# Kernel tuning notes

Hardware: AMD Instinct MI355X
Metric: run time of the kernel (lower is better)

Reference implementation:

```python
import jax, jax.numpy as jnp
import numpy as np

B, T, D, H, L, V = 2, 2048, 1024, 16, 12, 50257
HD = D // H          # head size 64
F = 4 * D            # FFN hidden 4096
EPS = 1e-5


def setup_inputs() -> dict:
    key = jax.random.key(0)
    keys = iter(jax.random.split(key, 16))
    n = lambda shape: jax.random.normal(next(keys), shape, jnp.float32) * 0.02
    inp = {
        "x": jax.random.randint(next(keys), (B, T), 0, V),
        "tok_emb": n((V, D)),
        "pos_emb": n((T, D)),
        "ln1_g": jnp.ones((L, D), jnp.float32), "ln1_b": jnp.zeros((L, D), jnp.float32),
        "wq": n((L, D, D)), "bq": jnp.zeros((L, D), jnp.float32),
        "wk": n((L, D, D)), "bk": jnp.zeros((L, D), jnp.float32),
        "wv": n((L, D, D)), "bv": jnp.zeros((L, D), jnp.float32),
        "wo": n((L, D, D)), "bo": jnp.zeros((L, D), jnp.float32),
        "ln2_g": jnp.ones((L, D), jnp.float32), "ln2_b": jnp.zeros((L, D), jnp.float32),
        "w1": n((L, D, F)), "b1": jnp.zeros((L, F), jnp.float32),
        "w2": n((L, F, D)), "b2": jnp.zeros((L, D), jnp.float32),
        "lnf_g": jnp.ones((D,), jnp.float32), "lnf_b": jnp.zeros((D,), jnp.float32),
        "fc_w": n((D, V)), "fc_b": jnp.zeros((V,), jnp.float32),
    }
    return inp


def _layernorm(x, g, b):
    m = jnp.mean(x, axis=-1, keepdims=True)
    v = jnp.var(x, axis=-1, keepdims=True)
    return (x - m) * jax.lax.rsqrt(v + EPS) * g + b


def _forward(x, tok_emb, pos_emb, ln1_g, ln1_b, wq, bq, wk, bk, wv, bv,
             wo, bo, ln2_g, ln2_b, w1, b1, w2, b2, lnf_g, lnf_b, fc_w, fc_b):
    # token + positional embedding (dropout is eval-mode identity)
    h = tok_emb[x] + pos_emb[None]                      # [B,T,D]
    mask = jnp.tril(jnp.ones((T, T), bool))             # causal mask
    scale = HD ** (-0.5)
    for l in range(L):
        # NOTE: original Block applies residual around the POST-norm activation
        hn = _layernorm(h, ln1_g[l], ln1_b[l])
        q = (hn @ wq[l] + bq[l]).reshape(B, T, H, HD)
        k = (hn @ wk[l] + bk[l]).reshape(B, T, H, HD)
        v = (hn @ wv[l] + bv[l]).reshape(B, T, H, HD)
        scores = jnp.einsum('bthd,bshd->bhts', q, k) * scale
        scores = jnp.where(mask[None, None], scores, -jnp.inf)
        attn = jax.nn.softmax(scores, axis=-1)
        o = jnp.einsum('bhts,bshd->bthd', attn, v).reshape(B, T, D)
        h = hn + (o @ wo[l] + bo[l])
        hn2 = _layernorm(h, ln2_g[l], ln2_b[l])
        h = hn2 + (jax.nn.relu(hn2 @ w1[l] + b1[l]) @ w2[l] + b2[l])
    h = _layernorm(h, lnf_g, lnf_b)
    logits = h @ fc_w + fc_b                            # [B,T,V]
    return logits


def reference(x, tok_emb, pos_emb, ln1_g, ln1_b, wq, bq, wk, bk, wv, bv,
              wo, bo, ln2_g, ln2_b, w1, b1, w2, b2, lnf_g, lnf_b, fc_w, fc_b):
    return _forward(x, tok_emb, pos_emb, ln1_g, ln1_b, wq, bq, wk, bk, wv, bv,
                    wo, bo, ln2_g, ln2_b, w1, b1, w2, b2, lnf_g, lnf_b, fc_w, fc_b)
```

## Files before the change

kernel.cpp:

```cpp
#include <hip/hip_runtime.h>

#define BB 2
#define TT 2048
#define DD 1024
#define HH 16
#define LL 12
#define VV 50257
#define VP 50432
#define HDD 64
#define FF 4096
#define MM (BB*TT)
#define QS 3072

typedef __bf16 bf16;
typedef __bf16 bf16x8 __attribute__((ext_vector_type(8)));
typedef __bf16 bf16x4 __attribute__((ext_vector_type(4)));
typedef __bf16 bf16x2 __attribute__((ext_vector_type(2)));
typedef float  f32x4  __attribute__((ext_vector_type(4)));
typedef float  f32x4u __attribute__((ext_vector_type(4), aligned(4)));
typedef unsigned int u32x4 __attribute__((ext_vector_type(4)));

typedef const __attribute__((address_space(1))) void* gas_t;
typedef __attribute__((address_space(3))) void* las_t;

__global__ __launch_bounds__(256) void k_embed(const int* __restrict__ x,
    const float* __restrict__ tok, const float* __restrict__ pos,
    float* __restrict__ h)
{
    int row = blockIdx.x;
    int t   = row & (TT - 1);
    int idx = x[row];
    int c   = threadIdx.x * 4;
    float4 a = *(const float4*)(tok + (size_t)idx * DD + c);
    float4 p = *(const float4*)(pos + (size_t)t   * DD + c);
    a.x += p.x; a.y += p.y; a.z += p.z; a.w += p.w;
    *(float4*)(h + (size_t)row * DD + c) = a;
}

__global__ __launch_bounds__(256) void k_ln(const float* __restrict__ in,
    const float* __restrict__ g, const float* __restrict__ b,
    float* __restrict__ outf, bf16* __restrict__ outb)
{
    int row = blockIdx.x, tid = threadIdx.x;
    const float4 v = *(const float4*)(in + (size_t)row * DD + tid * 4);
    float s  = v.x + v.y + v.z + v.w;
    float s2 = v.x*v.x + v.y*v.y + v.z*v.z + v.w*v.w;
    #pragma unroll
    for (int d = 1; d < 64; d <<= 1) { s += __shfl_xor(s, d); s2 += __shfl_xor(s2, d); }
    __shared__ float red[8];
    __shared__ float mv[2];
    int wid = tid >> 6, lane = tid & 63;
    if (lane == 0) { red[2*wid] = s; red[2*wid+1] = s2; }
    __syncthreads();
    if (tid == 0) {
        float ts  = red[0] + red[2] + red[4] + red[6];
        float ts2 = red[1] + red[3] + red[5] + red[7];
        float mean = ts * (1.0f / DD);
        float var  = ts2 * (1.0f / DD) - mean * mean;
        mv[0] = mean; mv[1] = 1.0f / sqrtf(var + 1e-5f);
    }
    __syncthreads();
    float mean = mv[0], inv = mv[1];
    float4 gg = *(const float4*)(g + tid * 4);
    float4 bb = *(const float4*)(b + tid * 4);
    float o0 = (v.x - mean) * inv * gg.x + bb.x;
    float o1 = (v.y - mean) * inv * gg.y + bb.y;
    float o2 = (v.z - mean) * inv * gg.z + bb.z;
    float o3 = (v.w - mean) * inv * gg.w + bb.w;
    size_t o = (size_t)row * DD + tid * 4;
    if (outf) { float4 r = {o0, o1, o2, o3}; *(float4*)(outf + o) = r; }
    if (outb) {
        bf16x4 r4 = {(bf16)o0, (bf16)o1, (bf16)o2, (bf16)o3};
        *(bf16x4*)(outb + o) = r4;
    }
}

__global__ __launch_bounds__(256) void k_wtrans(
    const float* __restrict__ src, bf16* __restrict__ dst,
    int K, int N, int Npad, size_t srcLS, size_t dstLS)
{
    src += (size_t)blockIdx.z * srcLS;
    dst += (size_t)blockIdx.z * dstLS;
    int k0 = blockIdx.y * 32, n0 = blockIdx.x * 256;
    __shared__ float tile[32][256];
    int tid = threadIdx.x;
    #pragma unroll
    for (int p = 0; p < 8; p++) {
        int kk = p * 4 + (tid >> 6);
        int nn = (tid & 63) * 4;
        const float* sp = src + (size_t)(k0 + kk) * N + n0 + nn;
        f32x4u v = {0.f, 0.f, 0.f, 0.f};
        if (n0 + nn + 3 < N) {
            v = *(const f32x4u*)sp;
        } else {
            #pragma unroll
            for (int i = 0; i < 4; i++)
                if (n0 + nn + i < N) v[i] = sp[i];
        }
        *(f32x4*)&tile[kk][nn] = v;
    }
    __syncthreads();
    int n = n0 + tid;
    if (n < Npad) {
        bf16 rowv[32];
        #pragma unroll
        for (int kk = 0; kk < 32; kk++) rowv[kk] = (bf16)tile[kk][tid];
        bf16* dp = dst + (size_t)n * K + k0;
        #pragma unroll
        for (int s = 0; s < 4; s++)
            *(bf16x8*)(dp + s * 8) = *(const bf16x8*)&rowv[s * 8];
    }
}

__global__ __launch_bounds__(256) void k_biasmerge(
    const float* __restrict__ bq, const float* __restrict__ bk,
    const float* __restrict__ bv, float* __restrict__ dst)
{
    int i = blockIdx.x * 256 + threadIdx.x;
    if (i >= LL * QS) return;
    int l = i / QS, j = i % QS;
    float v = (j < 1024) ? bq[l*1024 + j]
            : (j < 2048) ? bk[l*1024 + j - 1024]
                         : bv[l*1024 + j - 2048];
    dst[i] = v;
}

#define GEMM_EPILOGUE(MI_CNT, WM_STRIDE)                                        \
    bool nalign = ((Nout & 3) == 0);                                            \
    _Pragma("unroll")                                                           \
    for (int mi = 0; mi < MI_CNT; mi++) {                                       \
        int row = m0 + wm*WM_STRIDE + mi*16 + r16;                              \
        _Pragma("unroll")                                                       \
        for (int ni = 0; ni < 4; ni++) {                                        \
            int col0 = n0 + wn*64 + ni*16 + g4*4;                               \
            f32x4 v = acc[mi][ni];                                              \
            float sc = (qpre && col0 < 1024) ? 0.125f : 1.0f;                   \
            if (col0 + 3 < Nout) {                                              \
                if (bias) {                                                     \
                    float4 bi = *(const float4*)(bias + col0);                  \
                    v[0] += bi.x; v[1] += bi.y; v[2] += bi.z; v[3] += bi.w;     \
                }                                                               \
                if (res) {                                                      \
                    float4 rr = *(const float4*)(res + (size_t)row*Nout + col0);\
                    v[0] += rr.x; v[1] += rr.y; v[2] += rr.z; v[3] += rr.w;     \
                }                                                               \
                if (relu) { _Pragma("unroll")                                   \
                    for (int j = 0; j < 4; j++) v[j] = fmaxf(v[j], 0.0f); }     \
                if (outf) {                                                     \
                    float* p = outf + (size_t)row * Nout + col0;                \
                    if (nalign) *(f32x4*)p = v; else *(f32x4u*)p = v;           \
                }                                                               \
                if (outb) {                                                     \
                    bf16x4 o4 = {(bf16)(v[0]*sc), (bf16)(v[1]*sc),              \
                                 (bf16)(v[2]*sc), (bf16)(v[3]*sc)};             \
                    *(bf16x4*)(outb + (size_t)row * Nout + col0) = o4;          \
                }                                                               \
            } else {                                                            \
                _Pragma("unroll")                                               \
                for (int j = 0; j < 4; j++) {                                   \
                    int col = col0 + j;                                         \
                    if (col >= Nout) continue;                                  \
                    float vv = v[j] + (bias ? bias[col] : 0.0f);                \
                    if (res)  vv += res[(size_t)row * Nout + col];              \
                    if (relu) vv = fmaxf(vv, 0.0f);                             \
                    if (outf) outf[(size_t)row * Nout + col] = vv;              \
                    if (outb) outb[(size_t)row * Nout + col] = (bf16)(vv*sc);   \
                }                                                               \
            }                                                                   \
        }                                                                       \
    }


#define STG2(nn, kk)                                                            \
    do { const int k0_ = (nn)*64 + (kk)*32; const int db_ = (nn)&1;             \
        _Pragma("unroll") for (int i_ = 0; i_ < 2; i_++) {                      \
            int a_ = i_*2048 + tid*8;                                           \
            int sr_ = a_>>6, x_ = (a_&63) ^ ((sr_&7)<<3);                       \
            int r_ = 2*sr_ + (x_>>5), e_ = x_&31;                               \
            __builtin_amdgcn_global_load_lds(                                   \
                (gas_t)(A + (size_t)(m0+r_)*K + k0_+e_),                        \
                (las_t)&lA[db_][kk][a_], 16, 0, 0);                             \
        }                                                                       \
        _Pragma("unroll") for (int i_ = 0; i_ < 2; i_++) {                      \
            int a_ = i_*2048 + tid*8;                                           \
            int sr_ = a_>>6, x_ = (a_&63) ^ ((sr_&7)<<3);                       \
            int r_ = 2*sr_ + (x_>>5), e_ = x_&31;                               \
            __builtin_amdgcn_global_load_lds(                                   \
                (gas_t)(BT + (size_t)(n0+r_)*K + k0_+e_),                       \
                (las_t)&lB[db_][kk][a_], 16, 0, 0);                             \
        }                                                                       \
    } while (0)

#define PH2(nn, kk, sn, sk, wv)                                                 \
    { const int db_ = (nn)&1;                                                   \
        bf16x8 af[4], bfr[4];                                                   \
        _Pragma("unroll") for (int mi = 0; mi < 4; mi++) {                      \
            int row_ = wm*64 + mi*16 + r16;                                     \
            int sr_ = row_>>1;                                                  \
            int xp_ = (((row_&1)<<5) | kfrag) ^ ((sr_&7)<<3);                   \
            af[mi] = *(const bf16x8*)&lA[db_][kk][sr_*64 + xp_];                \
        }                                                                       \
        _Pragma("unroll") for (int ni = 0; ni < 4; ni++) {                      \
            int row_ = wn*64 + ni*16 + r16;                                     \
            int sr_ = row_>>1;                                                  \
            int xp_ = (((row_&1)<<5) | kfrag) ^ ((sr_&7)<<3);                   \
            bfr[ni] = *(const bf16x8*)&lB[db_][kk][sr_*64 + xp_];               \
        }                                                                       \
        bool st_ = (sn) < nt;                                                   \
        if (st_) STG2(sn, sk);                                                  \
        __builtin_amdgcn_sched_barrier(0);                                      \
        __builtin_amdgcn_s_barrier();                                           \
        __builtin_amdgcn_s_setprio(1);                                          \
        _Pragma("unroll") for (int mi = 0; mi < 4; mi++)                        \
            _Pragma("unroll") for (int ni = 0; ni < 4; ni++)                    \
                acc[mi][ni] = __builtin_amdgcn_mfma_f32_16x16x32_bf16(          \
                    bfr[ni], af[mi], acc[mi][ni], 0, 0, 0);                     \
        __builtin_amdgcn_s_setprio(0);                                          \
        if (wv) { if (st_) asm volatile("s_waitcnt vmcnt(4)" ::: "memory");     \
                  else     asm volatile("s_waitcnt vmcnt(0)" ::: "memory"); }   \
        __builtin_amdgcn_sched_barrier(0);                                      \
        __builtin_amdgcn_s_barrier();                                           \
    }

__global__ __launch_bounds__(256) void k_gemm2(
    const bf16* __restrict__ A, const bf16* __restrict__ BT,
    const float* __restrict__ bias, const float* __restrict__ res,
    float* __restrict__ outf, bf16* __restrict__ outb,
    int K, int Nout, int relu, int mswap, int qpre)
{
    __shared__ alignas(16) bf16 lA[2][2][128 * 32];
    __shared__ alignas(16) bf16 lB[2][2][128 * 32];
    int tid = threadIdx.x;
    int lane = tid & 63, w = tid >> 6;
    int wm = w >> 1, wn = w & 1;
    int nb = mswap ? blockIdx.y : blockIdx.x;
    int mb = mswap ? blockIdx.x : blockIdx.y;
    int n0 = nb * 128, m0 = mb * 128;
    int r16 = lane & 15, g4 = lane >> 4;
    int kfrag = g4 * 8;

    f32x4 acc[4][4];
    const f32x4 fzero = {0.f, 0.f, 0.f, 0.f};
    #pragma unroll
    for (int i = 0; i < 4; i++)
        #pragma unroll
        for (int j = 0; j < 4; j++) acc[i][j] = fzero;

    int nt = K >> 6;
    STG2(0, 0); STG2(0, 1); STG2(1, 0);
    asm volatile("s_waitcnt vmcnt(4)" ::: "memory");
    __builtin_amdgcn_sched_barrier(0);
    __builtin_amdgcn_s_barrier();
    for (int it2 = 0; it2 < nt; it2 += 2) {
        PH2(it2,     0, it2 + 1, 1, 0);
        PH2(it2,     1, it2 + 2, 0, 1);
        PH2(it2 + 1, 0, it2 + 2, 1, 0);
        PH2(it2 + 1, 1, it2 + 3, 0, 1);
    }
    GEMM_EPILOGUE(4, 64)
}

#define STG3(nn, kk)                                                            \
    do { const int k0_ = (nn)*64 + (kk)*32; const int db_ = (nn)&1;             \
        _Pragma("unroll") for (int i_ = 0; i_ < 2; i_++) {                      \
            int a_ = i_*4096 + tid*8;                                           \
            int sr_ = a_>>6, x_ = (a_&63) ^ ((sr_&7)<<3);                       \
            int r_ = 2*sr_ + (x_>>5), e_ = x_&31;                               \
            __builtin_amdgcn_global_load_lds(                                   \
                (gas_t)(A + (size_t)(m0+r_)*K + k0_+e_),                        \
                (las_t)&lA[db_][kk][a_], 16, 0, 0);                             \
        }                                                                       \
        _Pragma("unroll") for (int i_ = 0; i_ < 2; i_++) {                      \
            int a_ = i_*4096 + tid*8;                                           \
            int sr_ = a_>>6, x_ = (a_&63) ^ ((sr_&7)<<3);                       \
            int r_ = 2*sr_ + (x_>>5), e_ = x_&31;                               \
            __builtin_amdgcn_global_load_lds(                                   \
                (gas_t)(BT + (size_t)(n0+r_)*K + k0_+e_),                       \
                (las_t)&lB[db_][kk][a_], 16, 0, 0);                             \
        }                                                                       \
    } while (0)

#define PH3(nn, kk, sn, sk, wv)                                                 \
    { const int db_ = (nn)&1;                                                   \
        bf16x8 af[8], bfr[4];                                                   \
        _Pragma("unroll") for (int mi = 0; mi < 8; mi++) {                      \
            int row_ = wm*128 + mi*16 + r16;                                    \
            int sr_ = row_>>1;                                                  \
            int xp_ = (((row_&1)<<5) | kfrag) ^ ((sr_&7)<<3);                   \
            af[mi] = *(const bf16x8*)&lA[db_][kk][sr_*64 + xp_];                \
        }                                                                       \
        _Pragma("unroll") for (int ni = 0; ni < 4; ni++) {                      \
            int row_ = wn*64 + ni*16 + r16;                                     \
            int sr_ = row_>>1;                                                  \
            int xp_ = (((row_&1)<<5) | kfrag) ^ ((sr_&7)<<3);                   \
            bfr[ni] = *(const bf16x8*)&lB[db_][kk][sr_*64 + xp_];               \
        }                                                                       \
        bool st_ = (sn) < nt;                                                   \
        if (st_) STG3(sn, sk);                                                  \
        __builtin_amdgcn_sched_barrier(0);                                      \
        __builtin_amdgcn_s_barrier();                                           \
        __builtin_amdgcn_s_setprio(1);                                          \
        _Pragma("unroll") for (int mi = 0; mi < 8; mi++)                        \
            _Pragma("unroll") for (int ni = 0; ni < 4; ni++)                    \
                acc[mi][ni] = __builtin_amdgcn_mfma_f32_16x16x32_bf16(          \
                    bfr[ni], af[mi], acc[mi][ni], 0, 0, 0);                     \
        __builtin_amdgcn_s_setprio(0);                                          \
        if (wv) { if (st_) asm volatile("s_waitcnt vmcnt(4)" ::: "memory");     \
                  else     asm volatile("s_waitcnt vmcnt(0)" ::: "memory"); }   \
        __builtin_amdgcn_sched_barrier(0);                                      \
        __builtin_amdgcn_s_barrier();                                           \
    }

__global__ __launch_bounds__(512, 2) void k_gemm3(
    const bf16* __restrict__ A, const bf16* __restrict__ BT,
    const float* __restrict__ bias, const float* __restrict__ res,
    float* __restrict__ outf, bf16* __restrict__ outb,
    int K, int Nout, int relu, int mswap, int qpre)
{
    __shared__ alignas(16) bf16 lA[2][2][256 * 32];
    __shared__ alignas(16) bf16 lB[2][2][256 * 32];
    int tid = threadIdx.x;
    int lane = tid & 63, w = tid >> 6;
    int wm = w >> 2, wn = w & 3;
    int nb = mswap ? blockIdx.y : blockIdx.x;
    int mb = mswap ? blockIdx.x : blockIdx.y;
    int n0 = nb * 256, m0 = mb * 256;
    int r16 = lane & 15, g4 = lane >> 4;
    int kfrag = g4 * 8;

    f32x4 acc[8][4];
    const f32x4 fzero = {0.f, 0.f, 0.f, 0.f};
    #pragma unroll
    for (int i = 0; i < 8; i++)
        #pragma unroll
        for (int j = 0; j < 4; j++) acc[i][j] = fzero;

    int nt = K >> 6;
    STG3(0, 0); STG3(0, 1); STG3(1, 0);
    asm volatile("s_waitcnt vmcnt(4)" ::: "memory");
    __builtin_amdgcn_sched_barrier(0);
    __builtin_amdgcn_s_barrier();
    for (int it2 = 0; it2 < nt; it2 += 2) {
        PH3(it2,     0, it2 + 1, 1, 0);
        PH3(it2,     1, it2 + 2, 0, 1);
        PH3(it2 + 1, 0, it2 + 2, 1, 0);
        PH3(it2 + 1, 1, it2 + 3, 0, 1);
    }
    GEMM_EPILOGUE(8, 128)
}

__global__ __launch_bounds__(256) void k_gemm_f32b(
    const bf16* __restrict__ A, const float* __restrict__ Bm,
    const float* __restrict__ bias, float* __restrict__ outf,
    int M, int N, int K)
{
    __shared__ alignas(16) bf16 lA[128][40];
    __shared__ alignas(16) bf16 lB[128][40];
    int tid  = threadIdx.x;
    int lane = tid & 63, wid = tid >> 6;
    int wm = wid >> 1, wn = wid & 1;
    int m0 = blockIdx.x * 128, n0 = blockIdx.y * 128;
    int r16 = lane & 15, g4 = lane >> 4;

    f32x4 acc[4][4];
    const f32x4 fzero = {0.f, 0.f, 0.f, 0.f};
    #pragma unroll
    for (int i = 0; i < 4; i++)
        #pragma unroll
        for (int j = 0; j < 4; j++) acc[i][j] = fzero;

    int arow = tid >> 2, aseg = tid & 3;
    int bkr  = tid >> 3, bnb  = tid & 7;
    bool nfull = (n0 + 128 <= N);

    for (int k0 = 0; k0 < K; k0 += 32) {
        *(uint4*)&lA[arow][aseg*8] =
            *(const uint4*)(A + (size_t)(m0 + arow) * K + k0 + aseg*8);
        *(uint4*)&lA[arow + 64][aseg*8] =
            *(const uint4*)(A + (size_t)(m0 + arow + 64) * K + k0 + aseg*8);
        const float* bsrc = Bm + (size_t)(k0 + bkr) * N + n0;
        #pragma unroll
        for (int q = 0; q < 4; q++) {
            int n = q*32 + bnb*4;
            #pragma unroll
            for (int i = 0; i < 4; i++) {
                float fv = 0.0f;
                if (nfull || (n0 + n + i < N)) fv = bsrc[n + i];
                lB[n+i][bkr] = (bf16)fv;
            }
        }
        __syncthreads();
        int kb = g4 * 8;
        bf16x8 af[4], bfr[4];
        #pragma unroll
        for (int mi = 0; mi < 4; mi++)
            af[mi] = *(const bf16x8*)&lA[wm*64 + mi*16 + r16][kb];
        #pragma unroll
        for (int ni = 0; ni < 4; ni++)
            bfr[ni] = *(const bf16x8*)&lB[wn*64 + ni*16 + r16][kb];
        #pragma unroll
        for (int mi = 0; mi < 4; mi++)
            #pragma unroll
            for (int ni = 0; ni < 4; ni++)
                acc[mi][ni] = __builtin_amdgcn_mfma_f32_16x16x32_bf16(
                    af[mi], bfr[ni], acc[mi][ni], 0, 0, 0);
        __syncthreads();
    }

    #pragma unroll
    for (int ni = 0; ni < 4; ni++) {
        int col = n0 + wn*64 + ni*16 + r16;
        if (col >= N) continue;
        float bi = bias[col];
        #pragma unroll
        for (int mi = 0; mi < 4; mi++) {
            #pragma unroll
            for (int j = 0; j < 4; j++) {
                int row = m0 + wm*64 + mi*16 + g4*4 + j;
                outf[(size_t)row * N + col] = acc[mi][ni][j] + bi;
            }
        }
    }
}

__global__ __launch_bounds__(512) void k_attn3(
    const bf16* __restrict__ qkv, bf16* __restrict__ o)
{
    __shared__ alignas(16) bf16 lK[64][72];
    __shared__ alignas(16) bf16 lVT[64][72];
    int tid = threadIdx.x, lane = tid & 63, w = tid >> 6;
    int r16 = lane & 15, g4 = lane >> 4;
    int t0 = blockIdx.x * 128;
    int bh = blockIdx.y, bb = bh >> 4, hh = bh & 15;
    const bf16* base = qkv + (size_t)bb * TT * QS + hh * HDD;
    const bf16* kp = base + 1024;
    const bf16* vp = base + 2048;
    bf16* op = o + (size_t)bb * TT * DD + hh * HDD;
    int qrow = t0 + w * 16;

    bf16x8 qf0, qf1;
    {
        const bf16* qr = base + (size_t)(qrow + r16) * QS + g4 * 8;
        qf0 = *(const bf16x8*)qr;
        qf1 = *(const bf16x8*)(qr + 32);
    }

    int krow = tid >> 3, kseg = tid & 7;
    int vsp  = tid >> 4, vseg = tid & 15;

    f32x4 oacc[4];
    const f32x4 fzero = {0.f, 0.f, 0.f, 0.f};
    #pragma unroll
    for (int i = 0; i < 4; i++) oacc[i] = fzero;
    float mrun = -1e30f, lrun = 0.f;

    int send = t0 + 128;
    bf16x8 kr;
    bf16x4 va4, vb4;
    {
        kr  = *(const bf16x8*)(kp + (size_t)krow * QS + kseg * 8);
        va4 = *(const bf16x4*)(vp + (size_t)(2*vsp) * QS + vseg * 4);
        vb4 = *(const bf16x4*)(vp + (size_t)(2*vsp) * QS + QS + vseg * 4);
    }

    for (int s0 = 0; s0 < send; s0 += 64) {
        __syncthreads();
        *(bf16x8*)&lK[krow][kseg*8] = kr;
        #pragma unroll
        for (int i = 0; i < 4; i++) {
            int d = vseg*4 + i;
            int mpr = (vsp >> 2) ^ (d >> 3);
            bf16x2 pv2 = {va4[i], vb4[i]};
            *(unsigned int*)&lVT[d][mpr*8 + (vsp&3)*2] =
                __builtin_bit_cast(unsigned int, pv2);
        }
        if (s0 + 64 < send) {
            kr  = *(const bf16x8*)(kp + (size_t)(s0 + 64 + krow) * QS + kseg * 8);
            va4 = *(const bf16x4*)(vp + (size_t)(s0 + 64 + 2*vsp) * QS + vseg * 4);
            vb4 = *(const bf16x4*)(vp + (size_t)(s0 + 64 + 2*vsp) * QS + QS + vseg * 4);
        }
        __syncthreads();

        if (s0 <= qrow + 15) {
            f32x4 sf[4];
            __builtin_amdgcn_s_setprio(1);
            #pragma unroll
            for (int nf = 0; nf < 4; nf++) {
                sf[nf] = fzero;
                bf16x8 kf0 = *(const bf16x8*)&lK[nf*16 + r16][g4*8];
                bf16x8 kf1 = *(const bf16x8*)&lK[nf*16 + r16][32 + g4*8];
                sf[nf] = __builtin_amdgcn_mfma_f32_16x16x32_bf16(kf0, qf0, sf[nf], 0, 0, 0);
                sf[nf] = __builtin_amdgcn_mfma_f32_16x16x32_bf16(kf1, qf1, sf[nf], 0, 0, 0);
            }
            __builtin_amdgcn_s_setprio(0);
            int qa = qrow + r16;
            if (s0 + 63 > qrow) {
                #pragma unroll
                for (int nf = 0; nf < 4; nf++)
                    #pragma unroll
                    for (int j = 0; j < 4; j++)
                        if (s0 + nf*16 + g4*4 + j > qa) sf[nf][j] = -1e30f;
            }
            float pm = sf[0][0];
            #pragma unroll
            for (int nf = 0; nf < 4; nf++)
                #pragma unroll
                for (int j = 0; j < 4; j++) pm = fmaxf(pm, sf[nf][j]);
            pm = fmaxf(pm, __shfl_xor(pm, 16));
            pm = fmaxf(pm, __shfl_xor(pm, 32));
            float mn = fmaxf(mrun, pm);
            float al = __expf(mrun - mn);
            mrun = mn;
            float ps = 0.f;
            #pragma unroll
            for (int nf = 0; nf < 4; nf++)
                #pragma unroll
                for (int j = 0; j < 4; j++) {
                    float p = __expf(sf[nf][j] - mn);
                    sf[nf][j] = p;
                    ps += p;
                }
            ps += __shfl_xor(ps, 16);
            ps += __shfl_xor(ps, 32);
            lrun = lrun * al + ps;
            #pragma unroll
            for (int nf = 0; nf < 4; nf++)
                #pragma unroll
                for (int j = 0; j < 4; j++) oacc[nf][j] *= al;
            unsigned int pk[4][2];
            #pragma unroll
            for (int nf = 0; nf < 4; nf++) {
                bf16x2 a = {(bf16)sf[nf][0], (bf16)sf[nf][1]};
                bf16x2 b = {(bf16)sf[nf][2], (bf16)sf[nf][3]};
                pk[nf][0] = __builtin_bit_cast(unsigned int, a);
                pk[nf][1] = __builtin_bit_cast(unsigned int, b);
            }
            int srcA = r16 + (2*(g4 & 1))*16;
            int srcB = srcA + 16;
            bool hi2 = (g4 >= 2);
            __builtin_amdgcn_s_setprio(1);
            #pragma unroll
            for (int c = 0; c < 2; c++) {
                unsigned int a0 = __shfl(pk[2*c  ][0], srcA);
                unsigned int a1 = __shfl(pk[2*c+1][0], srcA);
                unsigned int b0 = __shfl(pk[2*c  ][1], srcA);
                unsigned int b1 = __shfl(pk[2*c+1][1], srcA);
                unsigned int e0 = __shfl(pk[2*c  ][0], srcB);
                unsigned int e1 = __shfl(pk[2*c+1][0], srcB);
                unsigned int f0 = __shfl(pk[2*c  ][1], srcB);
                unsigned int f1 = __shfl(pk[2*c+1][1], srcB);
                u32x4 uu = { hi2 ? a1 : a0, hi2 ? b1 : b0,
                             hi2 ? e1 : e0, hi2 ? f1 : f0 };
                bf16x8 pf = __builtin_bit_cast(bf16x8, uu);
                #pragma unroll
                for (int nf = 0; nf < 4; nf++) {
                    int d = nf*16 + r16;
                    int mread = (4*c + g4) ^ (d >> 3);
                    bf16x8 vt = *(const bf16x8*)&lVT[d][mread*8];
                    oacc[nf] = __builtin_amdgcn_mfma_f32_16x16x32_bf16(
                        vt, pf, oacc[nf], 0, 0, 0);
                }
            }
            __builtin_amdgcn_s_setprio(0);
        }
    }

    float inv = 1.0f / lrun;
    #pragma unroll
    for (int nf = 0; nf < 4; nf++) {
        f32x4 ov = oacc[nf];
        bf16x4 o4 = {(bf16)(ov[0]*inv), (bf16)(ov[1]*inv),
                     (bf16)(ov[2]*inv), (bf16)(ov[3]*inv)};
        *(bf16x4*)(op + (size_t)(qrow + r16) * DD + nf*16 + g4*4) = o4;
    }
}

extern "C" void kernel_launch(void* const* d_in, const int* in_sizes, int n_in,
                              void* d_out, int out_size, void* d_ws, size_t ws_size,
                              hipStream_t stream)
{
    (void)in_sizes; (void)n_in; (void)out_size;
    const int*   x    = (const int*)  d_in[0];
    const float* tok  = (const float*)d_in[1];
    const float* pos  = (const float*)d_in[2];
    const float* ln1g = (const float*)d_in[3];
    const float* ln1b = (const float*)d_in[4];
    const float* wq   = (const float*)d_in[5];
    const float* bq   = (const float*)d_in[6];
    const float* wk   = (const float*)d_in[7];
    const float* bk   = (const float*)d_in[8];
    const float* wv   = (const float*)d_in[9];
    const float* bv   = (const float*)d_in[10];
    const float* wo   = (const float*)d_in[11];
    const float* bo   = (const float*)d_in[12];
    const float* ln2g = (const float*)d_in[13];
    const float* ln2b = (const float*)d_in[14];
    const float* w1   = (const float*)d_in[15];
    const float* b1   = (const float*)d_in[16];
    const float* w2   = (const float*)d_in[17];
    const float* b2   = (const float*)d_in[18];
    const float* lnfg = (const float*)d_in[19];
    const float* lnfb = (const float*)d_in[20];
    const float* fcw  = (const float*)d_in[21];
    const float* fcb  = (const float*)d_in[22];

    const size_t MB = (size_t)1 << 20;
    char*  sb   = (char*)d_out;
    float* h    = (float*)(sb);
    float* hn   = (float*)(sb + 16*MB);
    bf16*  hnb  = (bf16*) (sb + 32*MB);
    bf16*  qkv  = (bf16*) (sb + 40*MB);
    bf16*  obuf = (bf16*) (sb + 64*MB);
    bf16*  f1b  = (bf16*) (sb + 72*MB);
    bf16*  WT   = (bf16*) (sb + 104*MB);
    float* bqkv = (float*)(sb + 392*MB);
    bf16*  hfb  = (bf16*) d_ws;

    const size_t LWT = 12582912;
    const size_t FCWT_BYTES = (size_t)VP * DD * 2;
    bool fast_logits = (ws_size >= 8*MB + FCWT_BYTES);
    bf16* fcwT = (bf16*)((char*)d_ws + 8*MB);

    dim3 blk(256);
    dim3 blk512(512);

    k_wtrans<<<dim3(4, 32, 12), blk, 0, stream>>>(wq, WT,               DD, DD, DD, (size_t)DD*DD, LWT);
    k_wtrans<<<dim3(4, 32, 12), blk, 0, stream>>>(wk, WT + 1024*1024,   DD, DD, DD, (size_t)DD*DD, LWT);
    k_wtrans<<<dim3(4, 32, 12), blk, 0, stream>>>(wv, WT + 2048*1024,   DD, DD, DD, (size_t)DD*DD, LWT);
    k_wtrans<<<dim3(4, 32, 12), blk, 0, stream>>>(wo, WT + 3145728,     DD, DD, DD, (size_t)DD*DD, LWT);
    k_wtrans<<<dim3(16, 32, 12), blk, 0, stream>>>(w1, WT + 4194304,    DD, FF, FF, (size_t)DD*FF, LWT);
    k_wtrans<<<dim3(4, 128, 12), blk, 0, stream>>>(w2, WT + 8388608,    FF, DD, DD, (size_t)FF*DD, LWT);
    if (fast_logits)
        k_wtrans<<<dim3(VP/256, 32, 1), blk, 0, stream>>>(fcw, fcwT, DD, VV, VP, 0, 0);
    k_biasmerge<<<dim3(144), blk, 0, stream>>>(bq, bk, bv, bqkv);

    k_embed<<<MM, blk, 0, stream>>>(x, tok, pos, h);
    for (int l = 0; l < LL; l++) {
        const bf16* WTl = WT + (size_t)l * LWT;
        k_ln<<<MM, blk, 0, stream>>>(h, ln1g + l*DD, ln1b + l*DD, hn, hnb);
        k_gemm2<<<dim3(24, 32), blk, 0, stream>>>(hnb, WTl, bqkv + l*QS,
                                                  nullptr, nullptr, qkv, DD, QS, 0, 0, 1);
        k_attn3<<<dim3(TT/128, BB*HH), blk512, 0, stream>>>(qkv, obuf);
        k_gemm2<<<dim3(8, 32), blk, 0, stream>>>(obuf, WTl + 3145728, bo + l*DD,
                                                 hn, h, nullptr, DD, DD, 0, 0, 0);
        k_ln<<<MM, blk, 0, stream>>>(h, ln2g + l*DD, ln2b + l*DD, hn, hnb);
        k_gemm3<<<dim3(FF/256, MM/256), blk512, 0, stream>>>(hnb, WTl + 4194304, b1 + l*FF,
                                                  nullptr, nullptr, f1b, DD, FF, 1, 0, 0);
        k_gemm2<<<dim3(8, 32), blk, 0, stream>>>(f1b, WTl + 8388608, b2 + l*DD,
                                                 hn, h, nullptr, FF, DD, 0, 0, 0);
    }
    k_ln<<<MM, blk, 0, stream>>>(h, lnfg, lnfb, nullptr, hfb);

    if (fast_logits) {
        k_gemm3<<<dim3(MM/256, VP/256), blk512, 0, stream>>>(hfb, fcwT, fcb,
                                                      nullptr, (float*)d_out, nullptr,
                                                      DD, VV, 0, 1, 0);
    } else {
        k_gemm_f32b<<<dim3(32, (VV + 127)/128), blk, 0, stream>>>(hfb, fcw, fcb,
                                                                  (float*)d_out, MM, VV, DD);
    }
}
```

Baseline: 4.546 ms.

## Restructure 256x256 GEMM staging into quadrant phases and defer softmax rescaling

The large-tile GEMM now stages whole 64-wide K tiles per buffer, with a row remap for B. It splits each tile's MFMA work into four quadrant phases, interleaving LDS fragment reads and global-to-LDS prefetches between barrier-separated compute blocks so memory traffic overlaps with matrix work at finer grain. Separately, the flash-attention softmax skips the running-max update and accumulator rescale when the wave-wide max grows by at most 8, trading a bounded exponent range for fewer exp and multiply operations. The extra barriers and more complex indexing add overhead and risk of mistakes.

```diff
diff --git a/kernel.cpp b/kernel.cpp
--- a/kernel.cpp
+++ b/kernel.cpp
@@ -170,6 +170,7 @@
         }                                                                       \
     }
 
+#define BARS { __builtin_amdgcn_sched_barrier(0); __builtin_amdgcn_s_barrier(); }
 
 #define STG2(nn, kk)                                                            \
     do { const int k0_ = (nn)*64 + (kk)*32; const int db_ = (nn)&1;             \
@@ -208,8 +209,7 @@
         }                                                                       \
         bool st_ = (sn) < nt;                                                   \
         if (st_) STG2(sn, sk);                                                  \
-        __builtin_amdgcn_sched_barrier(0);                                      \
-        __builtin_amdgcn_s_barrier();                                           \
+        BARS;                                                                   \
         __builtin_amdgcn_s_setprio(1);                                          \
         _Pragma("unroll") for (int mi = 0; mi < 4; mi++)                        \
             _Pragma("unroll") for (int ni = 0; ni < 4; ni++)                    \
@@ -218,8 +218,7 @@
         __builtin_amdgcn_s_setprio(0);                                          \
         if (wv) { if (st_) asm volatile("s_waitcnt vmcnt(4)" ::: "memory");     \
                   else     asm volatile("s_waitcnt vmcnt(0)" ::: "memory"); }   \
-        __builtin_amdgcn_sched_barrier(0);                                      \
-        __builtin_amdgcn_s_barrier();                                           \
+        BARS;                                                                   \
     }
 
 __global__ __launch_bounds__(256) void k_gemm2(
@@ -249,8 +248,7 @@
     int nt = K >> 6;
     STG2(0, 0); STG2(0, 1); STG2(1, 0);
     asm volatile("s_waitcnt vmcnt(4)" ::: "memory");
-    __builtin_amdgcn_sched_barrier(0);
-    __builtin_amdgcn_s_barrier();
+    BARS;
     for (int it2 = 0; it2 < nt; it2 += 2) {
         PH2(it2,     0, it2 + 1, 1, 0);
         PH2(it2,     1, it2 + 2, 0, 1);
@@ -260,56 +258,60 @@
     GEMM_EPILOGUE(4, 64)
 }
 
-#define STG3(nn, kk)                                                            \
-    do { const int k0_ = (nn)*64 + (kk)*32; const int db_ = (nn)&1;             \
-        _Pragma("unroll") for (int i_ = 0; i_ < 2; i_++) {                      \
-            int a_ = i_*4096 + tid*8;                                           \
-            int sr_ = a_>>6, x_ = (a_&63) ^ ((sr_&7)<<3);                       \
-            int r_ = 2*sr_ + (x_>>5), e_ = x_&31;                               \
-            __builtin_amdgcn_global_load_lds(                                   \
-                (gas_t)(A + (size_t)(m0+r_)*K + k0_+e_),                        \
-                (las_t)&lA[db_][kk][a_], 16, 0, 0);                             \
-        }                                                                       \
-        _Pragma("unroll") for (int i_ = 0; i_ < 2; i_++) {                      \
-            int a_ = i_*4096 + tid*8;                                           \
-            int sr_ = a_>>6, x_ = (a_&63) ^ ((sr_&7)<<3);                       \
-            int r_ = 2*sr_ + (x_>>5), e_ = x_&31;                               \
-            __builtin_amdgcn_global_load_lds(                                   \
-                (gas_t)(BT + (size_t)(n0+r_)*K + k0_+e_),                       \
-                (las_t)&lB[db_][kk][a_], 16, 0, 0);                             \
-        }                                                                       \
+#define SA3(tile, u)                                                            \
+    do { int s_ = tid*8; int rl_ = s_>>6;                                       \
+        int x_ = (s_&63) ^ ((rl_&7)<<3);                                        \
+        __builtin_amdgcn_global_load_lds(                                       \
+            (gas_t)(A + (size_t)(m0 + (u)*64 + rl_)*K + (size_t)(tile)*64 + x_),\
+            (las_t)&lA3[(tile)&1][(u)*4096 + s_], 16, 0, 0);                    \
     } while (0)
-
-#define PH3(nn, kk, sn, sk, wv)                                                 \
+#define SB3(tile, v)                                                            \
+    do { int s_ = tid*8; int rl_ = s_>>6; int lr_ = (v)*64 + rl_;               \
+        int r_ = (lr_ < 128) ? ((lr_&31) + ((lr_>>5)<<6))                       \
+                             : (32 + ((lr_-128)&31) + (((lr_-128)>>5)<<6));     \
+        int x_ = (s_&63) ^ ((rl_&7)<<3);                                        \
+        __builtin_amdgcn_global_load_lds(                                       \
+            (gas_t)(BT + (size_t)(n0 + r_)*K + (size_t)(tile)*64 + x_),         \
+            (las_t)&lB3[(tile)&1][(v)*4096 + s_], 16, 0, 0);                    \
+    } while (0)
+#define RDA3(dst, mig, mi, kh) { int lr_ = wm*128 + ((mig)*4+(mi))*16 + r16;    \
+    dst = *(const bf16x8*)&lA3[db_][lr_*64 + ((((kh)*32) | kfrag) ^ ((lr_&7)<<3))]; }
+#define RDB3(dst, ni, kh) { int lr_ = wn*32 + (((ni)&1)<<4) + r16 + (((ni)>=2)?128:0); \
+    dst = *(const bf16x8*)&lB3[db_][lr_*64 + ((((kh)*32) | kfrag) ^ ((lr_&7)<<3))]; }
+#define MF3(mb_, nb_)                                                           \
+    _Pragma("unroll") for (int kh = 0; kh < 2; kh++)                            \
+        _Pragma("unroll") for (int mi = 0; mi < 4; mi++)                        \
+            _Pragma("unroll") for (int ni = 0; ni < 2; ni++)                    \
+                acc[(mb_)+mi][(nb_)+ni] = __builtin_amdgcn_mfma_f32_16x16x32_bf16( \
+                    bfr[(nb_)+ni][kh], afr[mi][kh], acc[(mb_)+mi][(nb_)+ni], 0, 0, 0);
+
+#define QUAD3(nn, cs, sn)                                                       \
     { const int db_ = (nn)&1;                                                   \
-        bf16x8 af[8], bfr[4];                                                   \
-        _Pragma("unroll") for (int mi = 0; mi < 8; mi++) {                      \
-            int row_ = wm*128 + mi*16 + r16;                                    \
-            int sr_ = row_>>1;                                                  \
-            int xp_ = (((row_&1)<<5) | kfrag) ^ ((sr_&7)<<3);                   \
-            af[mi] = *(const bf16x8*)&lA[db_][kk][sr_*64 + xp_];                \
-        }                                                                       \
-        _Pragma("unroll") for (int ni = 0; ni < 4; ni++) {                      \
-            int row_ = wn*64 + ni*16 + r16;                                     \
-            int sr_ = row_>>1;                                                  \
-            int xp_ = (((row_&1)<<5) | kfrag) ^ ((sr_&7)<<3);                   \
-            bfr[ni] = *(const bf16x8*)&lB[db_][kk][sr_*64 + xp_];               \
-        }                                                                       \
-        bool st_ = (sn) < nt;                                                   \
-        if (st_) STG3(sn, sk);                                                  \
-        __builtin_amdgcn_sched_barrier(0);                                      \
-        __builtin_amdgcn_s_barrier();                                           \
-        __builtin_amdgcn_s_setprio(1);                                          \
-        _Pragma("unroll") for (int mi = 0; mi < 8; mi++)                        \
-            _Pragma("unroll") for (int ni = 0; ni < 4; ni++)                    \
-                acc[mi][ni] = __builtin_amdgcn_mfma_f32_16x16x32_bf16(          \
-                    bfr[ni], af[mi], acc[mi][ni], 0, 0, 0);                     \
-        __builtin_amdgcn_s_setprio(0);                                          \
-        if (wv) { if (st_) asm volatile("s_waitcnt vmcnt(4)" ::: "memory");     \
-                  else     asm volatile("s_waitcnt vmcnt(0)" ::: "memory"); }   \
-        __builtin_amdgcn_sched_barrier(0);                                      \
-        __builtin_amdgcn_s_barrier();                                           \
-    }
+                                                                        \
+      _Pragma("unroll") for (int mi=0;mi<4;mi++){RDA3(afr[mi][0],0,mi,0);RDA3(afr[mi][1],0,mi,1);} \
+      _Pragma("unroll") for (int ni=0;ni<2;ni++){RDB3(bfr[ni][0],ni,0);RDB3(bfr[ni][1],ni,1);}     \
+      BARS;                                                                     \
+      __builtin_amdgcn_s_setprio(1); MF3(0,0); __builtin_amdgcn_s_setprio(0);   \
+      BARS;                                                                     \
+                                                                        \
+      _Pragma("unroll") for (int ni=2;ni<4;ni++){RDB3(bfr[ni][0],ni,0);RDB3(bfr[ni][1],ni,1);}     \
+      if (cs) { SA3(sn,0); SA3(sn,2); }                                         \
+      BARS;                                                                     \
+      __builtin_amdgcn_s_setprio(1); MF3(0,2); __builtin_amdgcn_s_setprio(0);   \
+      BARS;                                                                     \
+                                                                        \
+      _Pragma("unroll") for (int mi=0;mi<4;mi++){RDA3(afr[mi][0],1,mi,0);RDA3(afr[mi][1],1,mi,1);} \
+      if (cs) { SB3(sn,0); SB3(sn,1); SB3(sn,2); SB3(sn,3); }                   \
+      BARS;                                                                     \
+      __builtin_amdgcn_s_setprio(1); MF3(4,0); __builtin_amdgcn_s_setprio(0);   \
+      BARS;                                                                     \
+                                                                        \
+      if (cs) { SA3(sn,1); SA3(sn,3); }                                         \
+      BARS;                                                                     \
+      __builtin_amdgcn_s_setprio(1); MF3(4,2); __builtin_amdgcn_s_setprio(0);   \
+      if (cs) asm volatile("s_waitcnt vmcnt(8)" ::: "memory");                  \
+      else    asm volatile("s_waitcnt vmcnt(0)" ::: "memory");                  \
+      BARS; }
 
 __global__ __launch_bounds__(512, 2) void k_gemm3(
     const bf16* __restrict__ A, const bf16* __restrict__ BT,
@@ -317,8 +319,8 @@
     float* __restrict__ outf, bf16* __restrict__ outb,
     int K, int Nout, int relu, int mswap, int qpre)
 {
-    __shared__ alignas(16) bf16 lA[2][2][256 * 32];
-    __shared__ alignas(16) bf16 lB[2][2][256 * 32];
+    __shared__ alignas(16) bf16 lA3[2][256 * 64];
+    __shared__ alignas(16) bf16 lB3[2][256 * 64];
     int tid = threadIdx.x;
     int lane = tid & 63, w = tid >> 6;
     int wm = w >> 2, wn = w & 3;
@@ -335,16 +337,20 @@
         #pragma unroll
         for (int j = 0; j < 4; j++) acc[i][j] = fzero;
 
+    bf16x8 afr[4][2];
+    bf16x8 bfr[4][2];
+
     int nt = K >> 6;
-    STG3(0, 0); STG3(0, 1); STG3(1, 0);
-    asm volatile("s_waitcnt vmcnt(4)" ::: "memory");
-    __builtin_amdgcn_sched_barrier(0);
-    __builtin_amdgcn_s_barrier();
+    SA3(0,0); SA3(0,1); SA3(0,2); SA3(0,3);
+    SB3(0,0); SB3(0,1); SB3(0,2); SB3(0,3);
+    SA3(1,0); SA3(1,1); SA3(1,2); SA3(1,3);
+    SB3(1,0); SB3(1,1); SB3(1,2); SB3(1,3);
+    asm volatile("s_waitcnt vmcnt(8)" ::: "memory");
+    BARS;
     for (int it2 = 0; it2 < nt; it2 += 2) {
-        PH3(it2,     0, it2 + 1, 1, 0);
-        PH3(it2,     1, it2 + 2, 0, 1);
-        PH3(it2 + 1, 0, it2 + 2, 1, 0);
-        PH3(it2 + 1, 1, it2 + 3, 0, 1);
+        bool c2 = (it2 + 2 < nt), c3 = (it2 + 3 < nt);
+        QUAD3(it2,     c2, it2 + 2);
+        QUAD3(it2 + 1, c3, it2 + 3);
     }
     GEMM_EPILOGUE(8, 128)
 }
@@ -508,25 +514,31 @@
                 for (int j = 0; j < 4; j++) pm = fmaxf(pm, sf[nf][j]);
             pm = fmaxf(pm, __shfl_xor(pm, 16));
             pm = fmaxf(pm, __shfl_xor(pm, 32));
-            float mn = fmaxf(mrun, pm);
-            float al = __expf(mrun - mn);
-            mrun = mn;
+            bool defer = (__all(pm - mrun <= 8.0f) != 0);
+            float al = 1.0f;
+            if (!defer) {
+                float mn = fmaxf(mrun, pm);
+                al = __expf(mrun - mn);
+                mrun = mn;
+            }
             float ps = 0.f;
             #pragma unroll
             for (int nf = 0; nf < 4; nf++)
                 #pragma unroll
                 for (int j = 0; j < 4; j++) {
-                    float p = __expf(sf[nf][j] - mn);
+                    float p = __expf(sf[nf][j] - mrun);
                     sf[nf][j] = p;
                     ps += p;
                 }
             ps += __shfl_xor(ps, 16);
             ps += __shfl_xor(ps, 32);
             lrun = lrun * al + ps;
-            #pragma unroll
-            for (int nf = 0; nf < 4; nf++)
+            if (!defer) {
                 #pragma unroll
-                for (int j = 0; j < 4; j++) oacc[nf][j] *= al;
+                for (int nf = 0; nf < 4; nf++)
+                    #pragma unroll
+                    for (int j = 0; j < 4; j++) oacc[nf][j] *= al;
+            }
             unsigned int pk[4][2];
             #pragma unroll
             for (int nf = 0; nf < 4; nf++) {
```

After: 4.498 ms. Within noise of the previous version (-1.1%).
